# Performance work log

Measured on AMD Instinct MI355X. Metric: run time of the kernel, lower is better.

Reference implementation:

```python
import jax, jax.numpy as jnp
import numpy as np

T, B, NS, NC = 64, 128, 64, 32
NSC = NS + NC


def setup_inputs() -> dict:
    key = jax.random.key(0)
    k0, k1, k2, k3, k4, k5 = jax.random.split(key, 6)
    # SPD quadratic cost: C = L L^T + I  (mpc.pytorch requires Quu > 0)
    L = 0.1 * jax.random.normal(k0, (T, B, NSC, NSC), jnp.float32)
    C = jnp.einsum('tbij,tbkj->tbik', L, L) + jnp.eye(NSC, dtype=jnp.float32)
    c = jax.random.normal(k1, (T, B, NSC), jnp.float32)
    # Stable linear dynamics: x+ = Fx x + Fu u + f
    Fx = 0.95 * jnp.eye(NS, dtype=jnp.float32) + 0.02 * jax.random.normal(k2, (T, B, NS, NS), jnp.float32)
    Fu = 0.1 * jax.random.normal(k3, (T, B, NS, NC), jnp.float32)
    F = jnp.concatenate([Fx, Fu], axis=-1)
    f = 0.1 * jax.random.normal(k4, (T, B, NS), jnp.float32)
    x_init = jax.random.normal(k5, (B, NS), jnp.float32)
    return {"C": C, "c": c, "F": F, "f": f, "x_init": x_init}


def _lqr(C, c, F, f, x_init):
    """Exact batched time-varying LQR (Riccati backward pass + rollout).

    This is the math of MPC.solve_lqr_subproblem for LinDx/QuadCost with no
    control bounds; with quadratic cost & linear dynamics one iLQR iteration
    (alpha=1) is the exact solution.
    Returns tau = [x; u] trajectory, shape [T, B, NS+NC].
    """
    n = x_init.shape[-1]
    b = x_init.shape[0]
    dt = C.dtype

    def bwd(carry, inp):
        V, v = carry                      # V: [B,n,n], v: [B,n]
        Ct, ct, Ft, ft = inp
        # Q = C + F^T V F ; q = c + F^T (V f + v)
        Q = Ct + jnp.einsum('bsi,bst,btj->bij', Ft, V, Ft)
        q = ct + jnp.einsum('bsi,bs->bi', Ft, v + jnp.einsum('bst,bt->bs', V, ft))
        Qxx, Qxu = Q[:, :n, :n], Q[:, :n, n:]
        Qux, Quu = Q[:, n:, :n], Q[:, n:, n:]
        qx, qu = q[:, :n], q[:, n:]
        # One solve for both feedback gain K and feedforward k
        Kk = -jnp.linalg.solve(Quu, jnp.concatenate([Qux, qu[..., None]], axis=-1))
        K, k = Kk[..., :n], Kk[..., n]    # K: [B,nc,n], k: [B,nc]
        Vn = (Qxx
              + jnp.einsum('bim,bmj->bij', Qxu, K)
              + jnp.einsum('bmi,bmj->bij', K, Qux)
              + jnp.einsum('bmi,bmn,bnj->bij', K, Quu, K))
        Vn = 0.5 * (Vn + jnp.swapaxes(Vn, -1, -2))
        vn = (qx
              + jnp.einsum('bim,bm->bi', Qxu, k)
              + jnp.einsum('bmi,bm->bi', K, qu + jnp.einsum('bmn,bn->bm', Quu, k)))
        return (Vn, vn), (K, k)

    V0 = jnp.zeros((b, n, n), dt)
    v0 = jnp.zeros((b, n), dt)
    _, (Ks, ks) = jax.lax.scan(bwd, (V0, v0), (C, c, F, f), reverse=True)

    def fwd(x, inp):
        K, k, Ft, ft = inp
        u = jnp.einsum('bmi,bi->bm', K, x) + k
        tau = jnp.concatenate([x, u], axis=-1)
        x_next = jnp.einsum('bsi,bi->bs', Ft, tau) + ft
        return x_next, tau

    _, taus = jax.lax.scan(fwd, x_init, (Ks, ks, F, f))
    return taus  # [T, B, NSC]


def reference(C, c, F, f, x_init):
    return _lqr(C, c, F, f, x_init)
```

## Files before the change

### kernel.cpp

```cpp
#include <hip/hip_runtime.h>


constexpr int T_   = 64;
constexpr int B_   = 128;
constexpr int NS_  = 64;
constexpr int NC_  = 32;
constexpr int NSC_ = 96;

constexpr int OFF_VS   = 0;
constexpr int OFF_WS   = 4352;
constexpr int OFF_QU   = 10752;
constexpr int OFF_SS   = 13952;
constexpr int OFF_LT   = 18304;
constexpr int OFF_INVD = 20416;
constexpr int OFF_QV   = 20480;
constexpr int OFF_HV   = 20580;
constexpr int OFF_VV   = 20644;
constexpr int OFF_XNB  = 20712;
constexpr int OFF_FB   = 20776;
constexpr int OFF_CU   = 33064;
constexpr int OFF_CF   = 36136;
constexpr int SMEM_F   = 37160;

typedef __attribute__((address_space(3))) void*       lds_vp;
typedef const __attribute__((address_space(1))) void* gas_vp;

__device__ __forceinline__ void g2l16(const float* g, float* l) {
  __builtin_amdgcn_global_load_lds((gas_vp)g, (lds_vp)l, 16, 0, 0);
}

__device__ __forceinline__ float rdlane(float v, int l) {
  return __builtin_bit_cast(float, __builtin_amdgcn_readlane(__builtin_bit_cast(int, v), l));
}

#define ASM_WAIT(S) asm volatile("s_waitcnt " S ::: "memory")
#define BAR()       __builtin_amdgcn_s_barrier()

__global__ __launch_bounds__(512) void lqr_all(
    const float* __restrict__ Cg, const float* __restrict__ cvg,
    const float* __restrict__ Fg, const float* __restrict__ fvg,
    const float* __restrict__ x0g, float* __restrict__ outg,
    float* __restrict__ Sws)
{
  const int b    = blockIdx.x;
  const int tid  = threadIdx.x;
  const int wid  = tid >> 6;
  const int lane = tid & 63;

  __shared__ float smem[SMEM_F];
  float (*Vs)[68]  = (float(*)[68]) (smem + OFF_VS);
  float (*Ws)[100] = (float(*)[100])(smem + OFF_WS);
  float (*Qu)[100] = (float(*)[100])(smem + OFF_QU);
  float* qv = smem + OFF_QV;
  float* hv = smem + OFF_HV;
  float* vv = smem + OFF_VV;

  for (int e = tid; e < 4352; e += 512) smem[e] = 0.f;
  if (tid < 64) vv[tid] = 0.f;

  auto backsolve = [&](int pb, size_t tbn, int col) {
    const float (*Sp)[68]  = (const float(*)[68])(smem + OFF_SS + pb * 2176);
    const float (*LTp)[33] = (const float(*)[33])(smem + OFF_LT + pb * 1056);
    const float* ivp = smem + OFF_INVD + pb * 32;
    float xr[32];
#pragma unroll
    for (int i = 0; i < 32; ++i) xr[i] = Sp[i][col];
#pragma unroll
    for (int i = 31; i >= 0; --i) {
      float v = xr[i];
#pragma unroll
      for (int k = i + 1; k < 32; ++k) v -= LTp[i][k] * xr[k];
      xr[i] = v * ivp[i];
    }
    float* Sg = Sws + tbn * 2080;
#pragma unroll
    for (int i = 0; i < 32; ++i) Sg[i * 65 + col] = xr[i];
  };

  {
    const size_t tb0 = (size_t)(T_ - 1) * B_ + b;
    const float* Fbase = Fg + tb0 * (NS_ * NSC_);
#pragma unroll
    for (int r = 0; r < 3; ++r) {
      const int q = wid * 3 + r;
      g2l16(Fbase + q * 256 + lane * 4, smem + OFF_FB + q * 256);
    }
    const int o = lane * 4;
    g2l16(cvg + tb0 * 96 + (o < 96 ? o : 92), smem + OFF_CF);
    g2l16(fvg + tb0 * 64 + (o < 64 ? o : 60), smem + OFF_CF + 256);
  }

  int cur = 0;

  const int tl   = (tid >= 256) ? (tid - 256) : 0;
  const int trow = (tl >> 3) * 2;
  const int tcol = (tl & 7) * 8;

  for (int t = T_ - 1; t >= 0; --t) {
    const size_t tb = (size_t)t * B_ + b;

    float4 cxa0, cxa1, cxb0, cxb1;

    {
      const float* CuB = Cg + tb * 9216 + 64 * 96;
      if (wid < 4) {
        g2l16(CuB + (wid * 2)     * 256 + lane * 4, smem + OFF_CU + (wid * 2)     * 256);
        g2l16(CuB + (wid * 2 + 1) * 256 + lane * 4, smem + OFF_CU + (wid * 2 + 1) * 256);
      } else {
        g2l16(CuB + (4 + wid) * 256 + lane * 4, smem + OFF_CU + (4 + wid) * 256);
        const float* Cb = Cg + tb * 9216;
        cxa0 = *(const float4*)(Cb + trow * 96 + tcol);
        cxa1 = *(const float4*)(Cb + trow * 96 + tcol + 4);
        cxb0 = *(const float4*)(Cb + (trow + 1) * 96 + tcol);
        cxb1 = *(const float4*)(Cb + (trow + 1) * 96 + tcol + 4);
      }
      const int tp = (t > 0) ? (t - 1) : 0;
      const size_t tbp = (size_t)tp * B_ + b;
      const float* Fbase = Fg + tbp * (NS_ * NSC_);
      float* fdst = smem + OFF_FB + (cur ^ 1) * 6144;
#pragma unroll
      for (int r = 0; r < 3; ++r) {
        const int q = wid * 3 + r;
        g2l16(Fbase + q * 256 + lane * 4, fdst + q * 256);
      }
      float* cdst = smem + OFF_CF + (cur ^ 1) * 512;
      const int o = lane * 4;
      g2l16(cvg + tbp * 96 + (o < 96 ? o : 92), cdst);
      g2l16(fvg + tbp * 64 + (o < 64 ? o : 60), cdst + 256);
    }

    if (wid < 4) { ASM_WAIT("vmcnt(7) lgkmcnt(0)"); } else { ASM_WAIT("vmcnt(10) lgkmcnt(0)"); }
    BAR();

    const float* Fb = smem + OFF_FB + cur * 6144;
    const float* cf = smem + OFF_CF + cur * 512;

    {
      const int s  = tid >> 3;
      const int j0 = (tid & 7) * 12;
      float a[12];
#pragma unroll
      for (int j = 0; j < 12; ++j) a[j] = 0.f;
#pragma unroll 4
      for (int u = 0; u < 64; ++u) {
        const float vu = Vs[u][s];
        const float4 b0 = *(const float4*)(Fb + u * 96 + j0);
        const float4 b1 = *(const float4*)(Fb + u * 96 + j0 + 4);
        const float4 b2 = *(const float4*)(Fb + u * 96 + j0 + 8);
        a[0] += vu * b0.x; a[1] += vu * b0.y; a[2]  += vu * b0.z; a[3]  += vu * b0.w;
        a[4] += vu * b1.x; a[5] += vu * b1.y; a[6]  += vu * b1.z; a[7]  += vu * b1.w;
        a[8] += vu * b2.x; a[9] += vu * b2.y; a[10] += vu * b2.z; a[11] += vu * b2.w;
      }
      *(float4*)&Ws[s][j0]     = make_float4(a[0], a[1], a[2],  a[3]);
      *(float4*)&Ws[s][j0 + 4] = make_float4(a[4], a[5], a[6],  a[7]);
      *(float4*)&Ws[s][j0 + 8] = make_float4(a[8], a[9], a[10], a[11]);
    }
    if (tid < 64) {
      float acc = vv[tid];
#pragma unroll 8
      for (int u = 0; u < 64; ++u) acc += Vs[u][tid] * cf[256 + u];
      hv[tid] = acc;
    }

    ASM_WAIT("vmcnt(5) lgkmcnt(0)");
    BAR();

    if (tid < 256) {
      const int i  = tid >> 3;
      const int j0 = (tid & 7) * 12;
      float a[12];
      {
        const float* cp = smem + OFF_CU + i * 96 + j0;
        const float4 c0 = *(const float4*)(cp);
        const float4 c1 = *(const float4*)(cp + 4);
        const float4 c2 = *(const float4*)(cp + 8);
        a[0] = c0.x; a[1] = c0.y; a[2]  = c0.z; a[3]  = c0.w;
        a[4] = c1.x; a[5] = c1.y; a[6]  = c1.z; a[7]  = c1.w;
        a[8] = c2.x; a[9] = c2.y; a[10] = c2.z; a[11] = c2.w;
      }
#pragma unroll 4
      for (int s2 = 0; s2 < 64; ++s2) {
        const float fu = Fb[s2 * 96 + 64 + i];
        const float4 w0 = *(const float4*)&Ws[s2][j0];
        const float4 w1 = *(const float4*)&Ws[s2][j0 + 4];
        const float4 w2 = *(const float4*)&Ws[s2][j0 + 8];
        a[0] += fu * w0.x; a[1] += fu * w0.y; a[2]  += fu * w0.z; a[3]  += fu * w0.w;
        a[4] += fu * w1.x; a[5] += fu * w1.y; a[6]  += fu * w1.z; a[7]  += fu * w1.w;
        a[8] += fu * w2.x; a[9] += fu * w2.y; a[10] += fu * w2.z; a[11] += fu * w2.w;
      }
      *(float4*)&Qu[i][j0]     = make_float4(a[0], a[1], a[2],  a[3]);
      *(float4*)&Qu[i][j0 + 4] = make_float4(a[4], a[5], a[6],  a[7]);
      *(float4*)&Qu[i][j0 + 8] = make_float4(a[8], a[9], a[10], a[11]);
    } else {
      float a0[8], a1[8];
      a0[0]=cxa0.x; a0[1]=cxa0.y; a0[2]=cxa0.z; a0[3]=cxa0.w;
      a0[4]=cxa1.x; a0[5]=cxa1.y; a0[6]=cxa1.z; a0[7]=cxa1.w;
      a1[0]=cxb0.x; a1[1]=cxb0.y; a1[2]=cxb0.z; a1[3]=cxb0.w;
      a1[4]=cxb1.x; a1[5]=cxb1.y; a1[6]=cxb1.z; a1[7]=cxb1.w;
#pragma unroll 4
      for (int u = 0; u < 64; ++u) {
        const float2 fx = *(const float2*)(Fb + u * 96 + trow);
        const float4 w0 = *(const float4*)&Ws[u][tcol];
        const float4 w1 = *(const float4*)&Ws[u][tcol + 4];
        a0[0] += fx.x * w0.x; a0[1] += fx.x * w0.y; a0[2] += fx.x * w0.z; a0[3] += fx.x * w0.w;
        a0[4] += fx.x * w1.x; a0[5] += fx.x * w1.y; a0[6] += fx.x * w1.z; a0[7] += fx.x * w1.w;
        a1[0] += fx.y * w0.x; a1[1] += fx.y * w0.y; a1[2] += fx.y * w0.z; a1[3] += fx.y * w0.w;
        a1[4] += fx.y * w1.x; a1[5] += fx.y * w1.y; a1[6] += fx.y * w1.z; a1[7] += fx.y * w1.w;
      }
      *(float4*)&Vs[trow][tcol]         = make_float4(a0[0], a0[1], a0[2], a0[3]);
      *(float4*)&Vs[trow][tcol + 4]     = make_float4(a0[4], a0[5], a0[6], a0[7]);
      *(float4*)&Vs[trow + 1][tcol]     = make_float4(a1[0], a1[1], a1[2], a1[3]);
      *(float4*)&Vs[trow + 1][tcol + 4] = make_float4(a1[4], a1[5], a1[6], a1[7]);
    }

    ASM_WAIT("lgkmcnt(0)");
    BAR();

    if (tid < 32) {
      const int i = tid;
      float a[32];
#pragma unroll
      for (int k = 0; k < 32; ++k) a[k] = Qu[i][64 + k];
      float (*LTc)[33] = (float(*)[33])(smem + OFF_LT + cur * 1056);
      float* ivc = smem + OFF_INVD + cur * 32;
#pragma unroll
      for (int j = 0; j < 32; ++j) {
        const float d   = rdlane(a[j], j);
        const float rin = 1.0f / sqrtf(d);
        const float l   = a[j] * rin;
        LTc[j][i] = l;
        if (i == 0) ivc[j] = rin;
#pragma unroll
        for (int k = j + 1; k < 32; ++k) {
          const float lkj = rdlane(l, k);
          a[k] = fmaf(-l, lkj, a[k]);
        }
      }
    } else if (tid >= 64 && tid <= 128) {
      if (t != T_ - 1) backsolve(cur ^ 1, (size_t)(t + 1) * B_ + b, tid - 64);
    } else if (tid >= 129 && tid < 225) {
      const int j = tid - 129;
      float acc = cf[j];
#pragma unroll 8
      for (int s2 = 0; s2 < 64; ++s2) acc += Fb[s2 * 96 + j] * hv[s2];
      qv[j] = acc;
    }

    ASM_WAIT("lgkmcnt(0)");
    BAR();

    if (tid < 65) {
      const float (*LTc)[33] = (const float(*)[33])(smem + OFF_LT + cur * 1056);
      const float* ivc = smem + OFF_INVD + cur * 32;
      float xr[32];
#pragma unroll
      for (int i = 0; i < 32; ++i) {
        float v = (tid < 64) ? Qu[i][tid] : qv[64 + i];
#pragma unroll
        for (int k = 0; k < i; ++k) v -= LTc[k][i] * xr[k];
        xr[i] = v * ivc[i];
      }
      float (*Sc)[68] = (float(*)[68])(smem + OFF_SS + cur * 2176);
#pragma unroll
      for (int i = 0; i < 32; ++i) Sc[i][tid] = xr[i];
    }

    ASM_WAIT("lgkmcnt(0)");
    BAR();

    {
      const int vi0 = (tid >> 4) * 2, vj0 = (tid & 15) * 4;
      const float (*Sc)[68] = (const float(*)[68])(smem + OFF_SS + cur * 2176);
      float p0[4] = {0.f, 0.f, 0.f, 0.f}, p1[4] = {0.f, 0.f, 0.f, 0.f};
#pragma unroll 4
      for (int m = 0; m < 32; ++m) {
        const float2 ya = *(const float2*)&Sc[m][vi0];
        const float4 yb = *(const float4*)&Sc[m][vj0];
        p0[0] += ya.x * yb.x; p0[1] += ya.x * yb.y; p0[2] += ya.x * yb.z; p0[3] += ya.x * yb.w;
        p1[0] += ya.y * yb.x; p1[1] += ya.y * yb.y; p1[2] += ya.y * yb.z; p1[3] += ya.y * yb.w;
      }
      float4 v0 = *(const float4*)&Vs[vi0][vj0];
      float4 v1 = *(const float4*)&Vs[vi0 + 1][vj0];
      v0.x -= p0[0]; v0.y -= p0[1]; v0.z -= p0[2]; v0.w -= p0[3];
      v1.x -= p1[0]; v1.y -= p1[1]; v1.z -= p1[2]; v1.w -= p1[3];
      *(float4*)&Vs[vi0][vj0]     = v0;
      *(float4*)&Vs[vi0 + 1][vj0] = v1;
    }
    if (tid < 64) {
      const float (*Sc)[68] = (const float(*)[68])(smem + OFF_SS + cur * 2176);
      float acc = qv[tid];
#pragma unroll 4
      for (int m = 0; m < 32; ++m) acc -= Sc[m][tid] * Sc[m][64];
      vv[tid] = acc;
    }

    ASM_WAIT("lgkmcnt(0)");
    BAR();
    cur ^= 1;
  }

  ASM_WAIT("vmcnt(0) lgkmcnt(0)");
  BAR();
  if (tid < 65) backsolve(1, (size_t)b, tid);
  ASM_WAIT("vmcnt(0) lgkmcnt(0)");
  BAR();

  float* tf  = smem + OFF_QV;
  float* xnb = smem + OFF_XNB;
  if (tid < 64) tf[tid] = x0g[(size_t)b * 64 + tid];

  auto stage_fwd = [&](int ts, int nb) {
    const size_t tbs = (size_t)ts * B_ + b;
    const float* Sb = Sws + tbs * 2080;
    float* sdst = smem + OFF_WS + nb * 2304;
#pragma unroll
    for (int r = 0; r < 2; ++r) {
      int q = wid * 2 + r; if (q > 8) q = 8;
      const int off = q * 256 + lane * 4;
      g2l16(Sb + (off < 2080 ? off : 2076), sdst + q * 256);
    }
    const float* Fbase = Fg + tbs * (NS_ * NSC_);
    float* fdst = smem + OFF_FB + nb * 6144;
#pragma unroll
    for (int r = 0; r < 3; ++r) {
      const int q = wid * 3 + r;
      g2l16(Fbase + q * 256 + lane * 4, fdst + q * 256);
    }
    const int o = lane * 4;
    g2l16(fvg + tbs * 64 + (o < 64 ? o : 60), smem + OFF_CF + nb * 512);
  };

  stage_fwd(0, 0);
  cur = 0;
  for (int t = 0; t < T_; ++t) {
    const size_t tb = (size_t)t * B_ + b;
    stage_fwd((t < T_ - 1) ? t + 1 : T_ - 1, cur ^ 1);
    ASM_WAIT("vmcnt(6) lgkmcnt(0)");
    BAR();

    if (tid < 256) {
      const int m = tid >> 3, l8 = tid & 7;
      const float* Sr = smem + OFF_WS + cur * 2304 + m * 65;
      float p = (l8 == 0) ? Sr[64] : 0.f;
      const int i0 = l8 * 8;
#pragma unroll
      for (int ii = 0; ii < 8; ++ii) p += Sr[i0 + ii] * tf[i0 + ii];
      p += __shfl_xor(p, 1); p += __shfl_xor(p, 2); p += __shfl_xor(p, 4);
      if (l8 == 0) tf[64 + m] = -p;
    }
    ASM_WAIT("lgkmcnt(0)");
    BAR();

    if (tid < 96) outg[tb * 96 + tid] = tf[tid];
    {
      const int s2 = tid >> 3, l8 = tid & 7;
      const float* Fr = smem + OFF_FB + cur * 6144 + s2 * 96 + l8 * 12;
      const float4 f0 = *(const float4*)(Fr);
      const float4 f1 = *(const float4*)(Fr + 4);
      const float4 f2 = *(const float4*)(Fr + 8);
      const int i0 = l8 * 12;
      float p = f0.x * tf[i0]     + f0.y * tf[i0 + 1] + f0.z * tf[i0 + 2]  + f0.w * tf[i0 + 3]
              + f1.x * tf[i0 + 4] + f1.y * tf[i0 + 5] + f1.z * tf[i0 + 6]  + f1.w * tf[i0 + 7]
              + f2.x * tf[i0 + 8] + f2.y * tf[i0 + 9] + f2.z * tf[i0 + 10] + f2.w * tf[i0 + 11];
      p += __shfl_xor(p, 1); p += __shfl_xor(p, 2); p += __shfl_xor(p, 4);
      if (l8 == 0) xnb[s2] = p + *(smem + OFF_CF + cur * 512 + s2);
    }
    ASM_WAIT("lgkmcnt(0)");
    BAR();
    if (tid < 64) tf[tid] = xnb[tid];
    cur ^= 1;
  }
}

extern "C" void kernel_launch(void* const* d_in, const int* in_sizes, int n_in,
                              void* d_out, int out_size, void* d_ws, size_t ws_size,
                              hipStream_t stream) {
  const float* C  = (const float*)d_in[0];
  const float* c  = (const float*)d_in[1];
  const float* F  = (const float*)d_in[2];
  const float* f  = (const float*)d_in[3];
  const float* x0 = (const float*)d_in[4];
  float* out = (float*)d_out;
  float* S   = (float*)d_ws;

  lqr_all<<<dim3(B_), dim3(512), 0, stream>>>(C, c, F, f, x0, out, S);
}
```

Measured before the change: 1.742 ms.

## Rebalance LQR Riccati and rollout work across warps with 4x4 register tiles

Reassigns the per-step matmuls (V·F, Quu/Qux, Vxx update, rank-32 downdate) to 4x4 register-blocked tiles spread over more threads, and moves the q-vector computation into an earlier phase. The backsolve is split across thread pairs with shuffles, and the Cholesky forward solve becomes right-looking. The last barrier of each backward step and the xnb staging buffer in the forward rollout are removed, and the x-part of F·tau is overlapped with the gain product. This is meant to shorten the serial critical path per timestep, at the cost of more intricate synchronisation and possible races around the removed barrier.

```diff
diff --git a/kernel.cpp b/kernel.cpp
--- a/kernel.cpp
+++ b/kernel.cpp
@@ -16,7 +16,6 @@
 constexpr int OFF_QV   = 20480;
 constexpr int OFF_HV   = 20580;
 constexpr int OFF_VV   = 20644;
-constexpr int OFF_XNB  = 20712;
 constexpr int OFF_FB   = 20776;
 constexpr int OFF_CU   = 33064;
 constexpr int OFF_CF   = 36136;
@@ -58,64 +57,85 @@
   for (int e = tid; e < 4352; e += 512) smem[e] = 0.f;
   if (tid < 64) vv[tid] = 0.f;
 
-  auto backsolve = [&](int pb, size_t tbn, int col) {
+  const int b_r4 = (tid & 15) * 4;
+  const int b_c4 = (tid >> 4) * 4;
+  const int q_i0 = (tid / 24) * 4;
+  const int q_j0 = (tid % 24) * 4;
+  const int tvs  = tid - 192;
+  const int v_r  = (tvs & 15) * 4;
+  const int v_c  = ((tvs >> 4) & 15) * 4;
+  const int tf2  = tid - 256;
+  const int f_i  = ((tf2 >> 4) & 15) * 4;
+  const int f_j  = (tf2 & 15) * 4;
+
+  auto backsolve2 = [&](int pb, size_t tbn) {
+    const int c = (tid - 128) >> 1;
+    const int h = (tid - 128) & 1;
     const float (*Sp)[68]  = (const float(*)[68])(smem + OFF_SS + pb * 2176);
     const float (*LTp)[33] = (const float(*)[33])(smem + OFF_LT + pb * 1056);
     const float* ivp = smem + OFF_INVD + pb * 32;
-    float xr[32];
-#pragma unroll
-    for (int i = 0; i < 32; ++i) xr[i] = Sp[i][col];
-#pragma unroll
-    for (int i = 31; i >= 0; --i) {
-      float v = xr[i];
-#pragma unroll
-      for (int k = i + 1; k < 32; ++k) v -= LTp[i][k] * xr[k];
-      xr[i] = v * ivp[i];
-    }
+    float r[16];
+#pragma unroll
+    for (int m = 0; m < 16; ++m) r[m] = Sp[2 * m + h][c];
     float* Sg = Sws + tbn * 2080;
 #pragma unroll
-    for (int i = 0; i < 32; ++i) Sg[i * 65 + col] = xr[i];
+    for (int k = 31; k >= 0; --k) {
+      const float cand  = r[k >> 1] * ivp[k];
+      const float other = __shfl_xor(cand, 1);
+      const float xk = ((k & 1) == h) ? cand : other;
+      if ((k & 1) == h) Sg[k * 65 + c] = xk;
+#pragma unroll
+      for (int m = 0; m <= (k - 1) >> 1; ++m) {
+        if (h < k - 2 * m)
+          r[m] -= LTp[2 * m + h][k] * xk;
+      }
+    }
   };
 
   {
     const size_t tb0 = (size_t)(T_ - 1) * B_ + b;
+    if (wid == 7) {
+      const int o = lane * 4;
+      g2l16(cvg + tb0 * 96 + (o < 96 ? o : 92), smem + OFF_CF);
+      g2l16(fvg + tb0 * 64 + (o < 64 ? o : 60), smem + OFF_CF + 256);
+    }
     const float* Fbase = Fg + tb0 * (NS_ * NSC_);
 #pragma unroll
     for (int r = 0; r < 3; ++r) {
       const int q = wid * 3 + r;
       g2l16(Fbase + q * 256 + lane * 4, smem + OFF_FB + q * 256);
     }
-    const int o = lane * 4;
-    g2l16(cvg + tb0 * 96 + (o < 96 ? o : 92), smem + OFF_CF);
-    g2l16(fvg + tb0 * 64 + (o < 64 ? o : 60), smem + OFF_CF + 256);
   }
 
   int cur = 0;
-
-  const int tl   = (tid >= 256) ? (tid - 256) : 0;
-  const int trow = (tl >> 3) * 2;
-  const int tcol = (tl & 7) * 8;
 
   for (int t = T_ - 1; t >= 0; --t) {
     const size_t tb = (size_t)t * B_ + b;
-
-    float4 cxa0, cxa1, cxb0, cxb1;
+    float4 cxa0 = {}, cxa1 = {}, cxb0 = {}, cxb1 = {};
 
     {
-      const float* CuB = Cg + tb * 9216 + 64 * 96;
-      if (wid < 4) {
-        g2l16(CuB + (wid * 2)     * 256 + lane * 4, smem + OFF_CU + (wid * 2)     * 256);
-        g2l16(CuB + (wid * 2 + 1) * 256 + lane * 4, smem + OFF_CU + (wid * 2 + 1) * 256);
-      } else {
-        g2l16(CuB + (4 + wid) * 256 + lane * 4, smem + OFF_CU + (4 + wid) * 256);
+      if (wid < 3) {
+        const float* CuB = Cg + tb * 9216 + 64 * 96;
+#pragma unroll
+        for (int r = 0; r < 4; ++r) {
+          const int q = wid * 4 + r;
+          g2l16(CuB + q * 256 + lane * 4, smem + OFF_CU + q * 256);
+        }
+      } else if (wid < 7) {
         const float* Cb = Cg + tb * 9216;
-        cxa0 = *(const float4*)(Cb + trow * 96 + tcol);
-        cxa1 = *(const float4*)(Cb + trow * 96 + tcol + 4);
-        cxb0 = *(const float4*)(Cb + (trow + 1) * 96 + tcol);
-        cxb1 = *(const float4*)(Cb + (trow + 1) * 96 + tcol + 4);
+        cxa0 = *(const float4*)(Cb + (v_r + 0) * 96 + v_c);
+        cxa1 = *(const float4*)(Cb + (v_r + 1) * 96 + v_c);
+        cxb0 = *(const float4*)(Cb + (v_r + 2) * 96 + v_c);
+        cxb1 = *(const float4*)(Cb + (v_r + 3) * 96 + v_c);
       }
       const int tp = (t > 0) ? (t - 1) : 0;
       const size_t tbp = (size_t)tp * B_ + b;
+      if (wid == 7) {
+        float* cdst = smem + OFF_CF + (cur ^ 1) * 512;
+        const int o = lane * 4;
+        g2l16(cvg + tbp * 96 + (o < 96 ? o : 92), cdst);
+        g2l16(fvg + tbp * 64 + (o < 64 ? o : 60), cdst + 256);
+      }
       const float* Fbase = Fg + tbp * (NS_ * NSC_);
       float* fdst = smem + OFF_FB + (cur ^ 1) * 6144;
 #pragma unroll
@@ -123,94 +143,106 @@
         const int q = wid * 3 + r;
         g2l16(Fbase + q * 256 + lane * 4, fdst + q * 256);
       }
-      float* cdst = smem + OFF_CF + (cur ^ 1) * 512;
-      const int o = lane * 4;
-      g2l16(cvg + tbp * 96 + (o < 96 ? o : 92), cdst);
-      g2l16(fvg + tbp * 64 + (o < 64 ? o : 60), cdst + 256);
-    }
-
-    if (wid < 4) { ASM_WAIT("vmcnt(7) lgkmcnt(0)"); } else { ASM_WAIT("vmcnt(10) lgkmcnt(0)"); }
+    }
+
+    if (wid == 7) { ASM_WAIT("vmcnt(5) lgkmcnt(0)"); }
+    else         { ASM_WAIT("vmcnt(7) lgkmcnt(0)"); }
     BAR();
 
     const float* Fb = smem + OFF_FB + cur * 6144;
     const float* cf = smem + OFF_CF + cur * 512;
 
-    {
-      const int s  = tid >> 3;
-      const int j0 = (tid & 7) * 12;
-      float a[12];
-#pragma unroll
-      for (int j = 0; j < 12; ++j) a[j] = 0.f;
+    if (tid < 384) {
+      float acc[4][4];
+#pragma unroll
+      for (int a2 = 0; a2 < 4; ++a2)
+#pragma unroll
+        for (int j = 0; j < 4; ++j) acc[a2][j] = 0.f;
 #pragma unroll 4
       for (int u = 0; u < 64; ++u) {
-        const float vu = Vs[u][s];
-        const float4 b0 = *(const float4*)(Fb + u * 96 + j0);
-        const float4 b1 = *(const float4*)(Fb + u * 96 + j0 + 4);
-        const float4 b2 = *(const float4*)(Fb + u * 96 + j0 + 8);
-        a[0] += vu * b0.x; a[1] += vu * b0.y; a[2]  += vu * b0.z; a[3]  += vu * b0.w;
-        a[4] += vu * b1.x; a[5] += vu * b1.y; a[6]  += vu * b1.z; a[7]  += vu * b1.w;
-        a[8] += vu * b2.x; a[9] += vu * b2.y; a[10] += vu * b2.z; a[11] += vu * b2.w;
-      }
-      *(float4*)&Ws[s][j0]     = make_float4(a[0], a[1], a[2],  a[3]);
-      *(float4*)&Ws[s][j0 + 4] = make_float4(a[4], a[5], a[6],  a[7]);
-      *(float4*)&Ws[s][j0 + 8] = make_float4(a[8], a[9], a[10], a[11]);
-    }
-    if (tid < 64) {
-      float acc = vv[tid];
-#pragma unroll 8
-      for (int u = 0; u < 64; ++u) acc += Vs[u][tid] * cf[256 + u];
-      hv[tid] = acc;
-    }
-
-    ASM_WAIT("vmcnt(5) lgkmcnt(0)");
-    BAR();
-
-    if (tid < 256) {
-      const int i  = tid >> 3;
-      const int j0 = (tid & 7) * 12;
-      float a[12];
-      {
-        const float* cp = smem + OFF_CU + i * 96 + j0;
-        const float4 c0 = *(const float4*)(cp);
-        const float4 c1 = *(const float4*)(cp + 4);
-        const float4 c2 = *(const float4*)(cp + 8);
-        a[0] = c0.x; a[1] = c0.y; a[2]  = c0.z; a[3]  = c0.w;
-        a[4] = c1.x; a[5] = c1.y; a[6]  = c1.z; a[7]  = c1.w;
-        a[8] = c2.x; a[9] = c2.y; a[10] = c2.z; a[11] = c2.w;
-      }
+        const float4 va = *(const float4*)&Vs[u][b_r4];
+        const float4 fb = *(const float4*)(Fb + u * 96 + b_c4);
+        const float av[4] = {va.x, va.y, va.z, va.w};
+        const float bv[4] = {fb.x, fb.y, fb.z, fb.w};
+#pragma unroll
+        for (int a2 = 0; a2 < 4; ++a2)
+#pragma unroll
+          for (int j = 0; j < 4; ++j) acc[a2][j] += av[a2] * bv[j];
+      }
+#pragma unroll
+      for (int a2 = 0; a2 < 4; ++a2)
+        *(float4*)&Ws[b_r4 + a2][b_c4] =
+            make_float4(acc[a2][0], acc[a2][1], acc[a2][2], acc[a2][3]);
+    } else if (tid < 448) {
+      const int s = tid - 384;
+      float acc = vv[s];
+#pragma unroll
+      for (int u4 = 0; u4 < 16; ++u4) {
+        const float4 vr = *(const float4*)&Vs[s][u4 * 4];
+        const float4 fr = *(const float4*)(cf + 256 + u4 * 4);
+        acc += vr.x * fr.x + vr.y * fr.y + vr.z * fr.z + vr.w * fr.w;
+      }
+      hv[s] = acc;
+    }
+
+    ASM_WAIT("vmcnt(3) lgkmcnt(0)");
+    BAR();
+
+    if (tid < 192) {
+      float a[4][4];
+#pragma unroll
+      for (int a2 = 0; a2 < 4; ++a2) {
+        const float4 cu = *(const float4*)(smem + OFF_CU + (q_i0 + a2) * 96 + q_j0);
+        a[a2][0] = cu.x; a[a2][1] = cu.y; a[a2][2] = cu.z; a[a2][3] = cu.w;
+      }
+#pragma unroll 4
+      for (int u = 0; u < 64; ++u) {
+        const float4 fu = *(const float4*)(Fb + u * 96 + 64 + q_i0);
+        const float4 w4 = *(const float4*)&Ws[u][q_j0];
+        const float av[4] = {fu.x, fu.y, fu.z, fu.w};
+        const float wv[4] = {w4.x, w4.y, w4.z, w4.w};
+#pragma unroll
+        for (int a2 = 0; a2 < 4; ++a2)
+#pragma unroll
+          for (int j = 0; j < 4; ++j) a[a2][j] += av[a2] * wv[j];
+      }
+#pragma unroll
+      for (int a2 = 0; a2 < 4; ++a2)
+        *(float4*)&Qu[q_i0 + a2][q_j0] =
+            make_float4(a[a2][0], a[a2][1], a[a2][2], a[a2][3]);
+    } else if (tid < 448) {
+      float a[4][4];
+      a[0][0] = cxa0.x; a[0][1] = cxa0.y; a[0][2] = cxa0.z; a[0][3] = cxa0.w;
+      a[1][0] = cxa1.x; a[1][1] = cxa1.y; a[1][2] = cxa1.z; a[1][3] = cxa1.w;
+      a[2][0] = cxb0.x; a[2][1] = cxb0.y; a[2][2] = cxb0.z; a[2][3] = cxb0.w;
+      a[3][0] = cxb1.x; a[3][1] = cxb1.y; a[3][2] = cxb1.z; a[3][3] = cxb1.w;
+#pragma unroll 4
+      for (int u = 0; u < 64; ++u) {
+        const float4 fx = *(const float4*)(Fb + u * 96 + v_r);
+        const float4 w4 = *(const float4*)&Ws[u][v_c];
+        const float av[4] = {fx.x, fx.y, fx.z, fx.w};
+        const float wv[4] = {w4.x, w4.y, w4.z, w4.w};
+#pragma unroll
+        for (int a2 = 0; a2 < 4; ++a2)
+#pragma unroll
+          for (int j = 0; j < 4; ++j) a[a2][j] += av[a2] * wv[j];
+      }
+#pragma unroll
+      for (int a2 = 0; a2 < 4; ++a2)
+        *(float4*)&Vs[v_r + a2][v_c] =
+            make_float4(a[a2][0], a[a2][1], a[a2][2], a[a2][3]);
+    } else {
+      const int j = tid - 448;
+      float acc0 = cf[j];
+      float acc1 = (j < 32) ? cf[64 + j] : 0.f;
 #pragma unroll 4
       for (int s2 = 0; s2 < 64; ++s2) {
-        const float fu = Fb[s2 * 96 + 64 + i];
-        const float4 w0 = *(const float4*)&Ws[s2][j0];
-        const float4 w1 = *(const float4*)&Ws[s2][j0 + 4];
-        const float4 w2 = *(const float4*)&Ws[s2][j0 + 8];
-        a[0] += fu * w0.x; a[1] += fu * w0.y; a[2]  += fu * w0.z; a[3]  += fu * w0.w;
-        a[4] += fu * w1.x; a[5] += fu * w1.y; a[6]  += fu * w1.z; a[7]  += fu * w1.w;
-        a[8] += fu * w2.x; a[9] += fu * w2.y; a[10] += fu * w2.z; a[11] += fu * w2.w;
-      }
-      *(float4*)&Qu[i][j0]     = make_float4(a[0], a[1], a[2],  a[3]);
-      *(float4*)&Qu[i][j0 + 4] = make_float4(a[4], a[5], a[6],  a[7]);
-      *(float4*)&Qu[i][j0 + 8] = make_float4(a[8], a[9], a[10], a[11]);
-    } else {
-      float a0[8], a1[8];
-      a0[0]=cxa0.x; a0[1]=cxa0.y; a0[2]=cxa0.z; a0[3]=cxa0.w;
-      a0[4]=cxa1.x; a0[5]=cxa1.y; a0[6]=cxa1.z; a0[7]=cxa1.w;
-      a1[0]=cxb0.x; a1[1]=cxb0.y; a1[2]=cxb0.z; a1[3]=cxb0.w;
-      a1[4]=cxb1.x; a1[5]=cxb1.y; a1[6]=cxb1.z; a1[7]=cxb1.w;
-#pragma unroll 4
-      for (int u = 0; u < 64; ++u) {
-        const float2 fx = *(const float2*)(Fb + u * 96 + trow);
-        const float4 w0 = *(const float4*)&Ws[u][tcol];
-        const float4 w1 = *(const float4*)&Ws[u][tcol + 4];
-        a0[0] += fx.x * w0.x; a0[1] += fx.x * w0.y; a0[2] += fx.x * w0.z; a0[3] += fx.x * w0.w;
-        a0[4] += fx.x * w1.x; a0[5] += fx.x * w1.y; a0[6] += fx.x * w1.z; a0[7] += fx.x * w1.w;
-        a1[0] += fx.y * w0.x; a1[1] += fx.y * w0.y; a1[2] += fx.y * w0.z; a1[3] += fx.y * w0.w;
-        a1[4] += fx.y * w1.x; a1[5] += fx.y * w1.y; a1[6] += fx.y * w1.z; a1[7] += fx.y * w1.w;
-      }
-      *(float4*)&Vs[trow][tcol]         = make_float4(a0[0], a0[1], a0[2], a0[3]);
-      *(float4*)&Vs[trow][tcol + 4]     = make_float4(a0[4], a0[5], a0[6], a0[7]);
-      *(float4*)&Vs[trow + 1][tcol]     = make_float4(a1[0], a1[1], a1[2], a1[3]);
-      *(float4*)&Vs[trow + 1][tcol + 4] = make_float4(a1[4], a1[5], a1[6], a1[7]);
+        const float hs = hv[s2];
+        acc0 += Fb[s2 * 96 + j] * hs;
+        if (j < 32) acc1 += Fb[s2 * 96 + 64 + j] * hs;
+      }
+      qv[j] = acc0;
+      if (j < 32) qv[64 + j] = acc1;
     }
 
     ASM_WAIT("lgkmcnt(0)");
@@ -236,14 +268,6 @@
           a[k] = fmaf(-l, lkj, a[k]);
         }
       }
-    } else if (tid >= 64 && tid <= 128) {
-      if (t != T_ - 1) backsolve(cur ^ 1, (size_t)(t + 1) * B_ + b, tid - 64);
-    } else if (tid >= 129 && tid < 225) {
-      const int j = tid - 129;
-      float acc = cf[j];
-#pragma unroll 8
-      for (int s2 = 0; s2 < 64; ++s2) acc += Fb[s2 * 96 + j] * hv[s2];
-      qv[j] = acc;
     }
 
     ASM_WAIT("lgkmcnt(0)");
@@ -252,61 +276,69 @@
     if (tid < 65) {
       const float (*LTc)[33] = (const float(*)[33])(smem + OFF_LT + cur * 1056);
       const float* ivc = smem + OFF_INVD + cur * 32;
-      float xr[32];
-#pragma unroll
-      for (int i = 0; i < 32; ++i) {
-        float v = (tid < 64) ? Qu[i][tid] : qv[64 + i];
-#pragma unroll
-        for (int k = 0; k < i; ++k) v -= LTc[k][i] * xr[k];
-        xr[i] = v * ivc[i];
+      float r[32];
+#pragma unroll
+      for (int i2 = 0; i2 < 32; ++i2)
+        r[i2] = (tid < 64) ? Qu[i2][tid] : qv[64 + i2];
+#pragma unroll
+      for (int i2 = 0; i2 < 32; ++i2) {
+        const float yi = r[i2] * ivc[i2];
+        r[i2] = yi;
+#pragma unroll
+        for (int k = i2 + 1; k < 32; ++k) r[k] -= LTc[i2][k] * yi;
       }
       float (*Sc)[68] = (float(*)[68])(smem + OFF_SS + cur * 2176);
 #pragma unroll
-      for (int i = 0; i < 32; ++i) Sc[i][tid] = xr[i];
+      for (int i2 = 0; i2 < 32; ++i2) Sc[i2][tid] = r[i2];
+    } else if (tid >= 128 && tid < 258) {
+      if (t != T_ - 1) backsolve2(cur ^ 1, (size_t)(t + 1) * B_ + b);
     }
 
     ASM_WAIT("lgkmcnt(0)");
     BAR();
 
     {
-      const int vi0 = (tid >> 4) * 2, vj0 = (tid & 15) * 4;
       const float (*Sc)[68] = (const float(*)[68])(smem + OFF_SS + cur * 2176);
-      float p0[4] = {0.f, 0.f, 0.f, 0.f}, p1[4] = {0.f, 0.f, 0.f, 0.f};
-#pragma unroll 4
-      for (int m = 0; m < 32; ++m) {
-        const float2 ya = *(const float2*)&Sc[m][vi0];
-        const float4 yb = *(const float4*)&Sc[m][vj0];
-        p0[0] += ya.x * yb.x; p0[1] += ya.x * yb.y; p0[2] += ya.x * yb.z; p0[3] += ya.x * yb.w;
-        p1[0] += ya.y * yb.x; p1[1] += ya.y * yb.y; p1[2] += ya.y * yb.z; p1[3] += ya.y * yb.w;
-      }
-      float4 v0 = *(const float4*)&Vs[vi0][vj0];
-      float4 v1 = *(const float4*)&Vs[vi0 + 1][vj0];
-      v0.x -= p0[0]; v0.y -= p0[1]; v0.z -= p0[2]; v0.w -= p0[3];
-      v1.x -= p1[0]; v1.y -= p1[1]; v1.z -= p1[2]; v1.w -= p1[3];
-      *(float4*)&Vs[vi0][vj0]     = v0;
-      *(float4*)&Vs[vi0 + 1][vj0] = v1;
-    }
-    if (tid < 64) {
-      const float (*Sc)[68] = (const float(*)[68])(smem + OFF_SS + cur * 2176);
-      float acc = qv[tid];
-#pragma unroll 4
-      for (int m = 0; m < 32; ++m) acc -= Sc[m][tid] * Sc[m][64];
-      vv[tid] = acc;
-    }
-
-    ASM_WAIT("lgkmcnt(0)");
-    BAR();
+      if (tid >= 256) {
+        float p[4][4];
+#pragma unroll
+        for (int a2 = 0; a2 < 4; ++a2)
+#pragma unroll
+          for (int j = 0; j < 4; ++j) p[a2][j] = 0.f;
+#pragma unroll 4
+        for (int m = 0; m < 32; ++m) {
+          const float4 ya = *(const float4*)&Sc[m][f_i];
+          const float4 yb = *(const float4*)&Sc[m][f_j];
+          const float av[4] = {ya.x, ya.y, ya.z, ya.w};
+          const float bv[4] = {yb.x, yb.y, yb.z, yb.w};
+#pragma unroll
+          for (int a2 = 0; a2 < 4; ++a2)
+#pragma unroll
+            for (int j = 0; j < 4; ++j) p[a2][j] += av[a2] * bv[j];
+        }
+#pragma unroll
+        for (int a2 = 0; a2 < 4; ++a2) {
+          float4 v4 = *(const float4*)&Vs[f_i + a2][f_j];
+          v4.x -= p[a2][0]; v4.y -= p[a2][1]; v4.z -= p[a2][2]; v4.w -= p[a2][3];
+          *(float4*)&Vs[f_i + a2][f_j] = v4;
+        }
+      } else if (tid < 64) {
+        float acc = qv[tid];
+#pragma unroll 4
+        for (int m = 0; m < 32; ++m) acc -= Sc[m][tid] * Sc[m][64];
+        vv[tid] = acc;
+      }
+    }
     cur ^= 1;
   }
 
   ASM_WAIT("vmcnt(0) lgkmcnt(0)");
   BAR();
-  if (tid < 65) backsolve(1, (size_t)b, tid);
+  if (tid >= 128 && tid < 258) backsolve2(1, (size_t)b);
   ASM_WAIT("vmcnt(0) lgkmcnt(0)");
   BAR();
 
-  float* tf  = smem + OFF_QV;
-  float* xnb = smem + OFF_XNB;
+  float* tf = smem + OFF_QV;
   if (tid < 64) tf[tid] = x0g[(size_t)b * 64 + tid];
 
   auto stage_fwd = [&](int ts, int nb) {
@@ -332,14 +364,27 @@
 
   stage_fwd(0, 0);
   cur = 0;
+  const int s4 = tid >> 2, l4 = tid & 3;
   for (int t = 0; t < T_; ++t) {
     const size_t tb = (size_t)t * B_ + b;
     stage_fwd((t < T_ - 1) ? t + 1 : T_ - 1, cur ^ 1);
     ASM_WAIT("vmcnt(6) lgkmcnt(0)");
     BAR();
 
+    const float* Fbc = smem + OFF_FB + cur * 6144;
+    float ax = 0.f;
+
+    if (tid < 64) outg[tb * 96 + tid] = tf[tid];
     if (tid < 256) {
-      const int m = tid >> 3, l8 = tid & 7;
+      const float* Fr = Fbc + s4 * 96 + l4 * 16;
+#pragma unroll
+      for (int q = 0; q < 4; ++q) {
+        const float4 fq = *(const float4*)(Fr + q * 4);
+        const float4 xq = *(const float4*)&tf[l4 * 16 + q * 4];
+        ax += fq.x * xq.x + fq.y * xq.y + fq.z * xq.z + fq.w * xq.w;
+      }
+    } else {
+      const int m = (tid - 256) >> 3, l8 = tid & 7;
       const float* Sr = smem + OFF_WS + cur * 2304 + m * 65;
       float p = (l8 == 0) ? Sr[64] : 0.f;
       const int i0 = l8 * 8;
@@ -351,23 +396,22 @@
     ASM_WAIT("lgkmcnt(0)");
     BAR();
 
-    if (tid < 96) outg[tb * 96 + tid] = tf[tid];
-    {
-      const int s2 = tid >> 3, l8 = tid & 7;
-      const float* Fr = smem + OFF_FB + cur * 6144 + s2 * 96 + l8 * 12;
-      const float4 f0 = *(const float4*)(Fr);
-      const float4 f1 = *(const float4*)(Fr + 4);
-      const float4 f2 = *(const float4*)(Fr + 8);
-      const int i0 = l8 * 12;
-      float p = f0.x * tf[i0]     + f0.y * tf[i0 + 1] + f0.z * tf[i0 + 2]  + f0.w * tf[i0 + 3]
-              + f1.x * tf[i0 + 4] + f1.y * tf[i0 + 5] + f1.z * tf[i0 + 6]  + f1.w * tf[i0 + 7]
-              + f2.x * tf[i0 + 8] + f2.y * tf[i0 + 9] + f2.z * tf[i0 + 10] + f2.w * tf[i0 + 11];
-      p += __shfl_xor(p, 1); p += __shfl_xor(p, 2); p += __shfl_xor(p, 4);
-      if (l8 == 0) xnb[s2] = p + *(smem + OFF_CF + cur * 512 + s2);
+    if (tid < 256) {
+      const float* Fu = Fbc + s4 * 96 + 64 + l4 * 8;
+      const float4 g0 = *(const float4*)(Fu);
+      const float4 g1 = *(const float4*)(Fu + 4);
+      const float4 u0 = *(const float4*)&tf[64 + l4 * 8];
+      const float4 u1 = *(const float4*)&tf[64 + l4 * 8 + 4];
+      float p = ax + g0.x * u0.x + g0.y * u0.y + g0.z * u0.z + g0.w * u0.w
+                   + g1.x * u1.x + g1.y * u1.y + g1.z * u1.z + g1.w * u1.w;
+      p += __shfl_xor(p, 1); p += __shfl_xor(p, 2);
+      if (l4 == 0) tf[s4] = p + *(smem + OFF_CF + cur * 512 + s4);
+    } else if (tid < 288) {
+      const int m = tid - 256;
+      outg[tb * 96 + 64 + m] = tf[64 + m];
     }
     ASM_WAIT("lgkmcnt(0)");
     BAR();
-    if (tid < 64) tf[tid] = xnb[tid];
     cur ^= 1;
   }
 }
```

Result: no change. 1.756 ms (+0.8%).
